# Kernel tuning notes

Hardware: AMD Instinct MI355X
Metric: run time of the kernel (lower is better)

The kernel has to match this reference:

```python
import jax, jax.numpy as jnp
import numpy as np

IMG_SIZE = 640
NUM_CLASSES = 80
KA = 3
STRIDES = (8, 16, 32)
CONF_THRESH = 0.001
NMS_THRESH = 0.6
ANCHORS = np.array([[12, 16], [19, 36], [40, 28],
                    [36, 75], [76, 55], [72, 146],
                    [142, 110], [192, 243], [459, 401]], np.float32).reshape(3, 3, 2)
CLS_OFFSET = 4.0  # > max normalized coord (1.0); separates classes for class-wise NMS


def _make_grid(stride):
    f = IMG_SIZE // stride
    gy, gx = jnp.meshgrid(jnp.arange(f), jnp.arange(f), indexing='ij')
    # [HW, 1, 2] in (x, y) order, row-major over (H, W) like permute(1,2,0).view(-1,...)
    return jnp.stack([gx, gy], axis=-1).reshape(-1, 1, 2).astype(jnp.float32)


def _decode_level(pred, level):
    # pred: [KA*(1+C+4), H, W] -> obj [HW*KA,1], cls [HW*KA,C], boxes [HW*KA,4]
    C = NUM_CLASSES
    p = jnp.transpose(pred, (1, 2, 0)).reshape(-1, KA * (1 + C + 4))  # [HW, ch]
    obj = p[:, :KA].reshape(-1, 1)
    cls = p[:, KA:KA * (1 + C)].reshape(-1, C)
    reg = p[:, KA * (1 + C):].reshape(-1, KA, 4)
    grid = _make_grid(STRIDES[level])               # [HW, 1, 2]
    anchors = jnp.asarray(ANCHORS[level])           # [KA, 2]
    xy = (jax.nn.sigmoid(reg[..., :2]) + grid) * STRIDES[level]
    wh = jnp.exp(reg[..., 2:]) * anchors
    box = jnp.concatenate([xy - wh * 0.5, xy + wh * 0.5], axis=-1).reshape(-1, 4)
    return obj, cls, box


def _greedy_nms(boxes, scores, valid, thresh):
    # Faithful sequential greedy NMS (same math as the numpy loop), via lax.scan.
    N = boxes.shape[0]
    order = jnp.argsort(-scores)
    b = boxes[order]
    v = valid[order]
    areas = (b[:, 2] - b[:, 0]) * (b[:, 3] - b[:, 1])
    idx = jnp.arange(N)

    def step(suppressed, i):
        keep_i = v[i] & jnp.logical_not(suppressed[i])
        xx1 = jnp.maximum(b[i, 0], b[:, 0])
        yy1 = jnp.maximum(b[i, 1], b[:, 1])
        xx2 = jnp.minimum(b[i, 2], b[:, 2])
        yy2 = jnp.minimum(b[i, 3], b[:, 3])
        w = jnp.maximum(1e-28, xx2 - xx1)
        h = jnp.maximum(1e-28, yy2 - yy1)
        inter = w * h
        ovr = inter / (areas[i] + areas - inter + 1e-14)
        suppressed = suppressed | (keep_i & (ovr > thresh) & (idx > i))
        return suppressed, keep_i

    _, kept_sorted = jax.lax.scan(step, jnp.zeros(N, bool), idx)
    return jnp.zeros(N, bool).at[order].set(kept_sorted)


def _forward(pred_s, pred_m, pred_l):
    outs = [_decode_level(p, i) for i, p in enumerate((pred_s, pred_m, pred_l))]
    obj = jnp.concatenate([o[0] for o in outs], axis=0)   # [N, 1]
    cls = jnp.concatenate([o[1] for o in outs], axis=0)   # [N, C]
    box = jnp.concatenate([o[2] for o in outs], axis=0)   # [N, 4]
    bboxes = jnp.clip(box / IMG_SIZE, 0.0, 1.0)
    scores = jax.nn.sigmoid(obj) * jax.nn.softmax(cls, axis=-1)  # [N, C]
    cls_inds = jnp.argmax(scores, axis=1)
    conf = jnp.max(scores, axis=1)
    valid = conf >= CONF_THRESH
    # per-class NMS == class-offset trick: different classes never overlap
    nms_boxes = bboxes + cls_inds.astype(bboxes.dtype)[:, None] * CLS_OFFSET
    keep = _greedy_nms(jax.lax.stop_gradient(nms_boxes),
                       jax.lax.stop_gradient(conf), valid, NMS_THRESH)
    return bboxes, conf, cls_inds, keep


def setup_inputs() -> dict:
    key = jax.random.key(0)
    k1, k2, k3 = jax.random.split(key, 3)
    ch = KA * (1 + NUM_CLASSES + 4)  # 255
    return {
        'pred_s': jax.random.normal(k1, (ch, 80, 80), jnp.float32),
        'pred_m': jax.random.normal(k2, (ch, 40, 40), jnp.float32),
        'pred_l': jax.random.normal(k3, (ch, 20, 20), jnp.float32),
    }


def reference(pred_s, pred_m, pred_l):
    # returns fixed-shape (bboxes [N,4], scores [N], cls_inds [N], keep mask [N])
    return _forward(pred_s, pred_m, pred_l)
```

## Files before the change

kernel.cpp:

```cpp
#include <hip/hip_runtime.h>

typedef unsigned long long u64;
typedef unsigned int u32;

#define NCLS 80
#define CAP 512
#define CNT_STRIDE 16
#define ST_STRIDE 36

__device__ __constant__ float c_AW[9] = {12.f,19.f,40.f,36.f,76.f,72.f,142.f,192.f,459.f};
__device__ __constant__ float c_AH[9] = {16.f,36.f,28.f,75.f,55.f,146.f,110.f,243.f,401.f};

__global__ __launch_bounds__(128)
void decode_kernel(const float* __restrict__ p0,
                   const float* __restrict__ p1,
                   const float* __restrict__ p2,
                   int* __restrict__ cnt,
                   u64* __restrict__ bucket,
                   float* __restrict__ out)
{
    const int bid = blockIdx.x;
    const float* p; int f, strd, base, lvl, rem;
    if (bid < 600)      { p = p0; f = 80; strd = 8;  base = 0;     lvl = 0; rem = bid; }
    else if (bid < 750) { p = p1; f = 40; strd = 16; base = 19200; lvl = 1; rem = bid - 600; }
    else                { p = p2; f = 20; strd = 32; base = 24000; lvl = 2; rem = bid - 750; }
    const int a    = rem % 3;
    const int tile = rem / 3;
    const int HW   = f * f;
    const int hw0  = tile << 5;

    __shared__ float st[88][ST_STRIDE];

    const int tid = threadIdx.x;

    {
        const int col = tid & 31;
        const int r0  = tid >> 5;
        const int hp  = min(hw0 + col, HW - 1);
        float vals[22];
        #pragma unroll
        for (int k = 0; k < 22; ++k) {
            const int row = r0 + 4 * k;
            if (row < 85) {
                const int ch = (row == 0) ? a
                             : (row <= 80 ? (3 + 80 * a + (row - 1))
                                          : (243 + 4 * a + (row - 81)));
                vals[k] = p[ch * HW + hp];
            }
        }
        #pragma unroll
        for (int k = 0; k < 22; ++k) {
            const int row = r0 + 4 * k;
            if (row < 85) st[row][col] = vals[k];
        }
    }
    __syncthreads();

    const int g = tid >> 2, q = tid & 3;
    const int cell = hw0 + g;
    if (cell >= HW) return;
    const int gx = cell % f;
    const int gy = cell / f;

    float v[20];
    #pragma unroll
    for (int k = 0; k < 20; ++k) v[k] = st[1 + 4 * k + q][g];

    float lmax = v[0];
    #pragma unroll
    for (int k = 1; k < 20; ++k) lmax = fmaxf(lmax, v[k]);
    float gm = lmax;
    gm = fmaxf(gm, __shfl_xor(gm, 1));
    gm = fmaxf(gm, __shfl_xor(gm, 2));

    float ls = 0.f, bp = -1.f; int ba_ = 0;
    #pragma unroll
    for (int k = 0; k < 20; ++k) {
        float pc = expf(v[k] - gm);
        ls += pc;
        if (pc > bp) { bp = pc; ba_ = 4 * k + q; }
    }
    float gs = ls;
    gs += __shfl_xor(gs, 1);
    gs += __shfl_xor(gs, 2);
    {
        float bp2 = __shfl_xor(bp, 1); int ba2 = __shfl_xor(ba_, 1);
        if (bp2 > bp || (bp2 == bp && ba2 < ba_)) { bp = bp2; ba_ = ba2; }
        bp2 = __shfl_xor(bp, 2); ba2 = __shfl_xor(ba_, 2);
        if (bp2 > bp || (bp2 == bp && ba2 < ba_)) { bp = bp2; ba_ = ba2; }
    }

    if (q != 0) return;

    float obj = st[0][g];
    float tx = st[81][g];
    float ty = st[82][g];
    float tw = st[83][g];
    float th = st[84][g];

    float sig  = 1.f / (1.f + expf(-obj));
    float conf = sig * (bp / gs);
    const int n = base + cell * 3 + a;

    if (conf >= 0.001f) {
        int pos = atomicAdd(&cnt[ba_ * CNT_STRIDE], 1);
        if (pos < CAP)
            bucket[ba_ * CAP + pos] = ((u64)__float_as_uint(conf) << 32) | (u64)(~(u32)n);
    }

    float sx = 1.f / (1.f + expf(-tx));
    float sy = 1.f / (1.f + expf(-ty));
    float cx = (sx + (float)gx) * (float)strd;
    float cy = (sy + (float)gy) * (float)strd;
    const int ai = lvl * 3 + a;
    float w  = expf(tw) * c_AW[ai];
    float h  = expf(th) * c_AH[ai];
    float hx = w * 0.5f, hy = h * 0.5f;
    float x1 = (cx - hx) / 640.0f;
    float y1 = (cy - hy) / 640.0f;
    float x2 = (cx + hx) / 640.0f;
    float y2 = (cy + hy) / 640.0f;
    x1 = fminf(fmaxf(x1, 0.f), 1.f);
    y1 = fminf(fmaxf(y1, 0.f), 1.f);
    x2 = fminf(fmaxf(x2, 0.f), 1.f);
    y2 = fminf(fmaxf(y2, 0.f), 1.f);

    *(float4*)(out + n * 4) = make_float4(x1, y1, x2, y2);
    out[100800 + n] = conf;
    out[126000 + n] = (float)ba_;
    out[151200 + n] = 0.0f;
}

__global__ __launch_bounds__(1024)
void nms_kernel(const int* __restrict__ cnt,
                const u64* __restrict__ bucket,
                const float* __restrict__ bboxes,
                float* __restrict__ out_keep)
{
    const int c = blockIdx.x;
    const int tid = threadIdx.x;
    const int wave = tid >> 6, lane = tid & 63;

    __shared__ float4 sbox[CAP + 1];
    __shared__ int    sgi[CAP];
    __shared__ u64    maskT[8 * CAP];

    const int M  = min(cnt[c * CNT_STRIDE], CAP);
    const int MW = (M + 63) >> 6;
    const u64* kb = bucket + c * CAP;

    if (wave < MW) {
        const int e = (wave << 6) + lane;
        if (e < M) {
            const u64 ke = kb[e];
            int rank = 0;
            int j = 0;
            for (; j + 8 <= M; j += 8) {
                rank += (int)(kb[j]   > ke) + (int)(kb[j+1] > ke)
                      + (int)(kb[j+2] > ke) + (int)(kb[j+3] > ke)
                      + (int)(kb[j+4] > ke) + (int)(kb[j+5] > ke)
                      + (int)(kb[j+6] > ke) + (int)(kb[j+7] > ke);
            }
            for (; j < M; ++j) rank += (int)(kb[j] > ke);

            const u32 gi = ~(u32)ke;
            const float4 b = *(const float4*)(bboxes + gi * 4);
            const float off = 4.0f * (float)c;
            sbox[rank] = make_float4(b.x + off, b.y + off, b.z + off, b.w + off);
            sgi[rank]  = (int)gi;
        }
    }
    __syncthreads();

    const int ntiles = (MW * (MW + 1)) >> 1;
    for (int t = wave; t < ntiles; t += 16) {
        int rw = 0, acc = 0;
        while (t >= acc + (MW - rw)) { acc += MW - rw; ++rw; }
        const int cw = rw + (t - acc);
        const int j  = (cw << 6) + lane;
        const float4 cb = sbox[min(j, M - 1)];
        const float  ca = (cb.z - cb.x) * (cb.w - cb.y);
        const int r0 = rw << 6;
        const int r1 = min(r0 + 64, M);
        u64 bits = 0ull;
        float4 nb = sbox[r0];
        for (int i = r0; i < r1; ++i) {
            const float4 rb = nb;
            nb = sbox[i + 1];
            const float ra = (rb.z - rb.x) * (rb.w - rb.y);
            float xx1 = fmaxf(rb.x, cb.x);
            float yy1 = fmaxf(rb.y, cb.y);
            float xx2 = fminf(rb.z, cb.z);
            float yy2 = fminf(rb.w, cb.w);
            float ww = fmaxf(1e-28f, xx2 - xx1);
            float hh = fmaxf(1e-28f, yy2 - yy1);
            float inter = ww * hh;
            float ovr = inter / (ra + ca - inter + 1e-14f);
            bits |= (u64)((i < j) && (ovr >= 0.6f)) << (i & 63);
        }
        maskT[rw * CAP + j] = bits;
    }
    __syncthreads();

    if (wave != 0) return;

    u64 k0 = 0, k1 = 0, k2 = 0, k3 = 0, k4 = 0, k5 = 0, k6 = 0, k7 = 0;
    (void)k7;
#define MT(W) maskT[(W) * CAP + j]
#define TILE(W, PRE)                                                    \
    if ((W) < MW) {                                                     \
        const int j = ((W) << 6) + lane;                                \
        const u64 mine = MT(W);                                         \
        const u64 pre = (PRE);                                          \
        const int rm = M - ((W) << 6);                                  \
        const u64 valid = (rm >= 64) ? ~0ull : ((1ull << rm) - 1ull);   \
        u64 cand = valid & ~__ballot(pre != 0ull);                      \
        u64 kept = 0ull;                                                \
        while (cand) {                                                  \
            const u64 remv = cand & __ballot((mine & kept) != 0ull);    \
            cand &= ~remv;                                              \
            const u64 newk = cand & __ballot((mine & cand) == 0ull);    \
            kept |= newk;                                               \
            cand &= ~newk;                                              \
        }                                                               \
        k##W = kept;                                                    \
        if ((kept >> lane) & 1ull) out_keep[sgi[j]] = 1.0f;             \
    }
    TILE(0, 0ull)
    TILE(1, (MT(0)&k0))
    TILE(2, (MT(0)&k0)|(MT(1)&k1))
    TILE(3, (MT(0)&k0)|(MT(1)&k1)|(MT(2)&k2))
    TILE(4, (MT(0)&k0)|(MT(1)&k1)|(MT(2)&k2)|(MT(3)&k3))
    TILE(5, (MT(0)&k0)|(MT(1)&k1)|(MT(2)&k2)|(MT(3)&k3)|(MT(4)&k4))
    TILE(6, (MT(0)&k0)|(MT(1)&k1)|(MT(2)&k2)|(MT(3)&k3)|(MT(4)&k4)|(MT(5)&k5))
    TILE(7, (MT(0)&k0)|(MT(1)&k1)|(MT(2)&k2)|(MT(3)&k3)|(MT(4)&k4)|(MT(5)&k5)|(MT(6)&k6))
#undef TILE
#undef MT
}

extern "C" void kernel_launch(void* const* d_in, const int* in_sizes, int n_in,
                              void* d_out, int out_size, void* d_ws, size_t ws_size,
                              hipStream_t stream) {
    const float* p0 = (const float*)d_in[0];
    const float* p1 = (const float*)d_in[1];
    const float* p2 = (const float*)d_in[2];
    float* out = (float*)d_out;

    char* ws = (char*)d_ws;
    int* cnt    = (int*)ws;
    u64* bucket = (u64*)(ws + 5120);

    hipMemsetAsync(cnt, 0, NCLS * CNT_STRIDE * sizeof(int), stream);
    decode_kernel<<<789, 128, 0, stream>>>(p0, p1, p2, cnt, bucket, out);
    nms_kernel<<<NCLS, 1024, 0, stream>>>(cnt, bucket, out, out + 151200);
}
```

Baseline: 51.92 us.

## Build per-class candidate lists inside NMS kernel instead of global atomics

Removes the memset launch and the global atomic bucketing from the decode kernel. Each NMS block now scans all 25200 conf/class entries from the output, collects its class's candidates into shared memory with shared atomics, and ranks them from LDS. This drops one launch and the global atomic contention. In exchange, each of the 80 blocks re-reads about 200KB of conf and class data.

Result: faster. 44.55 us (-14.2%).

```diff
diff --git a/kernel.cpp b/kernel.cpp
--- a/kernel.cpp
+++ b/kernel.cpp
@@ -5,7 +5,6 @@
 
 #define NCLS 80
 #define CAP 512
-#define CNT_STRIDE 16
 #define ST_STRIDE 36
 
 __device__ __constant__ float c_AW[9] = {12.f,19.f,40.f,36.f,76.f,72.f,142.f,192.f,459.f};
@@ -15,8 +14,6 @@
 void decode_kernel(const float* __restrict__ p0,
                    const float* __restrict__ p1,
                    const float* __restrict__ p2,
-                   int* __restrict__ cnt,
-                   u64* __restrict__ bucket,
                    float* __restrict__ out)
 {
     const int bid = blockIdx.x;
@@ -101,12 +98,6 @@
     float sig  = 1.f / (1.f + expf(-obj));
     float conf = sig * (bp / gs);
     const int n = base + cell * 3 + a;
-
-    if (conf >= 0.001f) {
-        int pos = atomicAdd(&cnt[ba_ * CNT_STRIDE], 1);
-        if (pos < CAP)
-            bucket[ba_ * CAP + pos] = ((u64)__float_as_uint(conf) << 32) | (u64)(~(u32)n);
-    }
 
     float sx = 1.f / (1.f + expf(-tx));
     float sy = 1.f / (1.f + expf(-ty));
@@ -132,39 +123,59 @@
 }
 
 __global__ __launch_bounds__(1024)
-void nms_kernel(const int* __restrict__ cnt,
-                const u64* __restrict__ bucket,
-                const float* __restrict__ bboxes,
+void nms_kernel(const float* __restrict__ out,
                 float* __restrict__ out_keep)
 {
     const int c = blockIdx.x;
     const int tid = threadIdx.x;
     const int wave = tid >> 6, lane = tid & 63;
 
+    __shared__ int    scnt;
+    __shared__ u64    skey[CAP];
     __shared__ float4 sbox[CAP + 1];
     __shared__ int    sgi[CAP];
     __shared__ u64    maskT[8 * CAP];
 
-    const int M  = min(cnt[c * CNT_STRIDE], CAP);
+    if (tid == 0) scnt = 0;
+    __syncthreads();
+
+    const float* confp = out + 100800;
+    const float* clsp  = out + 126000;
+    for (int ib = tid; ib < 6300; ib += 1024) {
+        const float4 cf4 = *(const float4*)(confp + ib * 4);
+        const float4 cl4 = *(const float4*)(clsp  + ib * 4);
+        #pragma unroll
+        for (int k = 0; k < 4; ++k) {
+            const float cf = (k == 0) ? cf4.x : (k == 1) ? cf4.y : (k == 2) ? cf4.z : cf4.w;
+            const float cl = (k == 0) ? cl4.x : (k == 1) ? cl4.y : (k == 2) ? cl4.z : cl4.w;
+            if ((int)cl == c && cf >= 0.001f) {
+                const int i = ib * 4 + k;
+                const int pos = atomicAdd(&scnt, 1);
+                if (pos < CAP)
+                    skey[pos] = ((u64)__float_as_uint(cf) << 32) | (u64)(~(u32)i);
+            }
+        }
+    }
+    __syncthreads();
+    const int M  = min(scnt, CAP);
     const int MW = (M + 63) >> 6;
-    const u64* kb = bucket + c * CAP;
 
     if (wave < MW) {
         const int e = (wave << 6) + lane;
         if (e < M) {
-            const u64 ke = kb[e];
+            const u64 ke = skey[e];
             int rank = 0;
             int j = 0;
             for (; j + 8 <= M; j += 8) {
-                rank += (int)(kb[j]   > ke) + (int)(kb[j+1] > ke)
-                      + (int)(kb[j+2] > ke) + (int)(kb[j+3] > ke)
-                      + (int)(kb[j+4] > ke) + (int)(kb[j+5] > ke)
-                      + (int)(kb[j+6] > ke) + (int)(kb[j+7] > ke);
+                rank += (int)(skey[j]   > ke) + (int)(skey[j+1] > ke)
+                      + (int)(skey[j+2] > ke) + (int)(skey[j+3] > ke)
+                      + (int)(skey[j+4] > ke) + (int)(skey[j+5] > ke)
+                      + (int)(skey[j+6] > ke) + (int)(skey[j+7] > ke);
             }
-            for (; j < M; ++j) rank += (int)(kb[j] > ke);
+            for (; j < M; ++j) rank += (int)(skey[j] > ke);
 
             const u32 gi = ~(u32)ke;
-            const float4 b = *(const float4*)(bboxes + gi * 4);
+            const float4 b = *(const float4*)(out + gi * 4);
             const float off = 4.0f * (float)c;
             sbox[rank] = make_float4(b.x + off, b.y + off, b.z + off, b.w + off);
             sgi[rank]  = (int)gi;
@@ -246,11 +257,6 @@
     const float* p2 = (const float*)d_in[2];
     float* out = (float*)d_out;
 
-    char* ws = (char*)d_ws;
-    int* cnt    = (int*)ws;
-    u64* bucket = (u64*)(ws + 5120);
-
-    hipMemsetAsync(cnt, 0, NCLS * CNT_STRIDE * sizeof(int), stream);
-    decode_kernel<<<789, 128, 0, stream>>>(p0, p1, p2, cnt, bucket, out);
-    nms_kernel<<<NCLS, 1024, 0, stream>>>(cnt, bucket, out, out + 151200);
+    decode_kernel<<<789, 128, 0, stream>>>(p0, p1, p2, out);
+    nms_kernel<<<NCLS, 1024, 0, stream>>>(out, out + 151200);
 }
```
